# Optimization experiments

Measured on AMD Instinct MI355X. Metric: run time of the kernel, lower is better.

Reference implementation:

```python
import jax, jax.numpy as jnp
import numpy as np

EPS = 1e-5

def conv2d(x, w, padding):
    # x: (N, Cin, H, W), w: (Cout, Cin, kh, kw)
    return jax.lax.conv_general_dilated(
        x, w, window_strides=(1, 1),
        padding=[(padding, padding), (padding, padding)],
        dimension_numbers=('NCHW', 'OIHW', 'NCHW'))

def proj_bn_relu(x, w, gamma, beta, mean, var):
    # 1x1 conv + BatchNorm (eval mode, running stats) + ReLU
    y = conv2d(x, w, 0)
    scale = (gamma / jnp.sqrt(var + EPS))[None, :, None, None]
    shift = (beta - mean * gamma / jnp.sqrt(var + EPS))[None, :, None, None]
    return jax.nn.relu(y * scale + shift)

def setup_inputs() -> dict:
    key = jax.random.key(0)
    ks = jax.random.split(key, 16)
    B, Sx, Sy, C1, C2, Co, H, W, K = 2, 4, 4, 64, 64, 64, 128, 128, 3
    inp = {
        'u': jax.random.normal(ks[0], (B, Sx, C1, H, W), jnp.float32),
        'v': jax.random.normal(ks[1], (B, Sy, C2, H, W), jnp.float32),
        'pu_w': jax.random.normal(ks[2], (C1, C1, 1, 1), jnp.float32) * 0.05,
        'pu_gamma': jnp.ones((C1,), jnp.float32),
        'pu_beta': jnp.zeros((C1,), jnp.float32),
        'pu_mean': jax.random.normal(ks[3], (C1,), jnp.float32) * 0.1,
        'pu_var': jax.random.uniform(ks[4], (C1,), jnp.float32, 0.5, 1.5),
        'pv_w': jax.random.normal(ks[5], (C2, C2, 1, 1), jnp.float32) * 0.05,
        'pv_gamma': jnp.ones((C2,), jnp.float32),
        'pv_beta': jnp.zeros((C2,), jnp.float32),
        'pv_mean': jax.random.normal(ks[6], (C2,), jnp.float32) * 0.1,
        'pv_var': jax.random.uniform(ks[7], (C2,), jnp.float32, 0.5, 1.5),
        'conv_w': jax.random.normal(ks[8], (Co, C1 + C2, K, K), jnp.float32) * 0.02,
        'conv_b': jax.random.normal(ks[9], (Co,), jnp.float32) * 0.02,
    }
    return inp

def reference(u, v, pu_w, pu_gamma, pu_beta, pu_mean, pu_var,
              pv_w, pv_gamma, pv_beta, pv_mean, pv_var, conv_w, conv_b):
    B, Sx, C1, H, W = u.shape
    _, Sy, C2, _, _ = v.shape
    pad = 1
    # flatten set dims into batch for the 1x1 proj+BN+ReLU
    uf = proj_bn_relu(u.reshape(B * Sx, C1, H, W), pu_w, pu_gamma, pu_beta, pu_mean, pu_var)
    vf = proj_bn_relu(v.reshape(B * Sy, C2, H, W), pv_w, pv_gamma, pv_beta, pv_mean, pv_var)
    # conv over concat channels is linear -> split weight and broadcast-add,
    # exactly equal to conv(cat(repeat(u), repeat(v))) without materializing
    # the (B,Sx,Sy,C1+C2,H,W) tensor.
    w_u = conv_w[:, :C1]   # (Co, C1, K, K)
    w_v = conv_w[:, C1:]   # (Co, C2, K, K)
    ou = conv2d(uf, w_u, pad)  # (B*Sx, Co, Ho, Wo)
    ov = conv2d(vf, w_v, pad)  # (B*Sy, Co, Ho, Wo)
    Co, Ho, Wo = ou.shape[1], ou.shape[2], ou.shape[3]
    ou = ou.reshape(B, Sx, 1, Co, Ho, Wo)
    ov = ov.reshape(B, 1, Sy, Co, Ho, Wo)
    out = ou + ov + conv_b[None, None, None, :, None, None]
    return out  # (B, Sx, Sy, Co, Ho, Wo)
```

## Files before the change

kernel.cpp:

```cpp
#include <hip/hip_runtime.h>
#include <hip/hip_bf16.h>

#define C   64
#define Hh  128
#define Ww  128
#define HW  16384

typedef __attribute__((ext_vector_type(8))) short bf16x8;
typedef __attribute__((ext_vector_type(4))) float f32x4;

__device__ __forceinline__ unsigned short f2bf(float f) {
    unsigned u = __builtin_bit_cast(unsigned, f);
    unsigned r = (u + 0x7fff + ((u >> 16) & 1)) >> 16;
    return (unsigned short)r;
}

__global__ __launch_bounds__(256) void prep_kernel(
    const float* __restrict__ pu_w, const float* __restrict__ pu_g,
    const float* __restrict__ pu_b, const float* __restrict__ pu_m,
    const float* __restrict__ pu_v,
    const float* __restrict__ pv_w, const float* __restrict__ pv_g,
    const float* __restrict__ pv_b, const float* __restrict__ pv_m,
    const float* __restrict__ pv_v,
    const float* __restrict__ conv_w,
    short* __restrict__ pwu, short* __restrict__ pwv,
    short* __restrict__ wpu, short* __restrict__ wpv,
    float* __restrict__ shu, float* __restrict__ shv)
{
    const int idx = blockIdx.x * 256 + threadIdx.x;
    if (idx < 8192) {
        const int c  = idx >> 12;
        const int r  = idx & 4095;
        const int co = r >> 6, ci = r & 63;
        const float* w = c ? pv_w : pu_w;
        const float* g = c ? pv_g : pu_g;
        const float* vv = c ? pv_v : pu_v;
        const float scale = g[co] * rsqrtf(vv[co] + 1e-5f);
        (c ? pwv : pwu)[r] = (short)f2bf(w[co * 64 + ci] * scale);
    } else if (idx < 81920) {
        const int flat = idx - 8192;
        const int c  = flat / 36864;
        const int r  = flat % 36864;
        const int ch  = r / 18432;
        const int r2  = r % 18432;
        const int tap = r2 / 2048;
        const int r3  = r2 & 2047;
        const int co = r3 >> 5, ci = r3 & 31;
        const float src = conv_w[(size_t)(co * 128 + c * 64 + ch * 32 + ci) * 9 + tap];
        (c ? wpv : wpu)[((ch * 9 + tap) * 64 + co) * 32 + ci] = (short)f2bf(src);
    } else if (idx < 82048) {
        const int r  = idx - 81920;
        const int c  = r >> 6, co = r & 63;
        const float* g = c ? pv_g : pu_g;
        const float* b = c ? pv_b : pu_b;
        const float* m = c ? pv_m : pu_m;
        const float* vv = c ? pv_v : pu_v;
        const float scale = g[co] * rsqrtf(vv[co] + 1e-5f);
        (c ? shv : shu)[co] = b[co] - m[co] * scale;
    }
}

__global__ __launch_bounds__(256) void proj_mfma(
    const float* __restrict__ xu, const float* __restrict__ xv,
    const short* __restrict__ pwu_, const short* __restrict__ pwv_,
    const float* __restrict__ shu_, const float* __restrict__ shv_,
    short* __restrict__ yu, short* __restrict__ yv)
{
    __shared__ short xs[256 * 72];
    __shared__ short pwl[64 * 72];
    __shared__ float ssh[64];

    const int img16 = blockIdx.y;
    const int sel   = img16 >> 3;
    const int img   = img16 & 7;
    const float* x      = sel ? xv   : xu;
    const short* pw     = sel ? pwv_ : pwu_;
    const float* shiftg = sel ? shv_ : shu_;
    short* y            = sel ? yv   : yu;

    const int pix0 = blockIdx.x * 256;
    const int tid  = threadIdx.x;

    const float* xi = x + (size_t)img * C * HW + pix0 + tid;
#pragma unroll 8
    for (int c2 = 0; c2 < 32; ++c2) {
        const float a = xi[(size_t)(2 * c2) * HW];
        const float b = xi[(size_t)(2 * c2 + 1) * HW];
        const int packed = (int)f2bf(a) | ((int)f2bf(b) << 16);
        *(int*)(&xs[tid * 72 + c2 * 2]) = packed;
    }
#pragma unroll
    for (int it = 0; it < 2; ++it) {
        const int idx = tid + it * 256;
        const int oct = idx & 7, co = idx >> 3;
        *(int4*)(&pwl[co * 72 + oct * 8]) = *(const int4*)(&pw[co * 64 + oct * 8]);
    }
    if (tid < 64) ssh[tid] = shiftg[tid];
    __syncthreads();

    const int wq = tid >> 6;
    const int lane = tid & 63;
    const int lx = lane & 15;
    const int q  = lane >> 4;

    f32x4 acc[4][4];
#pragma unroll
    for (int mt = 0; mt < 4; ++mt)
#pragma unroll
        for (int nt = 0; nt < 4; ++nt) acc[mt][nt] = (f32x4){0.f, 0.f, 0.f, 0.f};

#pragma unroll
    for (int kc = 0; kc < 2; ++kc) {
        bf16x8 a[4], b[4];
#pragma unroll
        for (int mt = 0; mt < 4; ++mt)
            a[mt] = *(const bf16x8*)&xs[((wq * 4 + mt) * 16 + lx) * 72 + kc * 32 + q * 8];
#pragma unroll
        for (int nt = 0; nt < 4; ++nt)
            b[nt] = *(const bf16x8*)&pwl[(nt * 16 + lx) * 72 + kc * 32 + q * 8];
#pragma unroll
        for (int mt = 0; mt < 4; ++mt)
#pragma unroll
            for (int nt = 0; nt < 4; ++nt)
                acc[mt][nt] = __builtin_amdgcn_mfma_f32_16x16x32_bf16(a[mt], b[nt], acc[mt][nt], 0, 0, 0);
    }

    short* yo = y + ((size_t)img * HW + pix0) * C;
#pragma unroll
    for (int mt = 0; mt < 4; ++mt)
#pragma unroll
        for (int nt = 0; nt < 4; ++nt)
#pragma unroll
            for (int r = 0; r < 4; ++r) {
                const int pixl = (wq * 4 + mt) * 16 + q * 4 + r;
                const int co = nt * 16 + lx;
                float vv = acc[mt][nt][r] + ssh[co];
                vv = fmaxf(vv, 0.f);
                yo[(size_t)pixl * C + co] = (short)f2bf(vv);
            }
}

template<bool FUSED>
__global__ __launch_bounds__(256, 2) void conv_core(
    const short* __restrict__ act, const short* __restrict__ wp,
    const float* __restrict__ ou, const float* __restrict__ bias,
    float* __restrict__ outp)
{
    __shared__ short xs[340 * 40];
    __shared__ short wsm[9 * 64 * 40];
    __shared__ float sbias[64];

    const int img = blockIdx.y;
    const int tx = blockIdx.x & 3, ty = blockIdx.x >> 2;
    const int h0 = ty * 8, w0 = tx * 32;
    const int tid = threadIdx.x;
    const int wq = tid >> 6;
    const int lane = tid & 63;
    const int lx = lane & 15;
    const int q8 = (lane >> 4) * 8;

    if (FUSED && tid < 64) sbias[tid] = bias[tid];

    f32x4 acc[4][4];
#pragma unroll
    for (int mt = 0; mt < 4; ++mt)
#pragma unroll
        for (int nt = 0; nt < 4; ++nt) acc[mt][nt] = (f32x4){0.f, 0.f, 0.f, 0.f};

    const short* ub = act + (size_t)img * HW * C;

    for (int ch = 0; ch < 2; ++ch) {
        __syncthreads();
        for (int idx = tid; idx < 1360; idx += 256) {
            const int oct = idx & 3;
            const int pcell = idx >> 2;
            const int h = pcell / 34, w = pcell - h * 34;
            const int gh = h0 - 1 + h, gw = w0 - 1 + w;
            int4 v = {0, 0, 0, 0};
            if (gh >= 0 && gh < Hh && gw >= 0 && gw < Ww)
                v = *(const int4*)&ub[(size_t)(gh * Ww + gw) * C + ch * 32 + oct * 8];
            *(int4*)(&xs[pcell * 40 + oct * 8]) = v;
        }
        for (int idx = tid; idx < 2304; idx += 256) {
            const int oct = idx & 3;
            const int co = (idx >> 2) & 63;
            const int tl = idx >> 8;
            *(int4*)(&wsm[(tl * 64 + co) * 40 + oct * 8]) =
                *(const int4*)&wp[(((ch * 9 + tl) * 64) + co) * 32 + oct * 8];
        }
        __syncthreads();
#pragma unroll
        for (int t = 0; t < 9; ++t) {
            const int ky = t / 3;
            const int kx = t - ky * 3;
            bf16x8 a[4], b[4];
#pragma unroll
            for (int mt = 0; mt < 4; ++mt)
                a[mt] = *(const bf16x8*)&wsm[(t * 64 + mt * 16 + lx) * 40 + q8];
#pragma unroll
            for (int nt = 0; nt < 4; ++nt) {
                const int cell = (2 * wq + (nt >> 1) + ky) * 34 + (nt & 1) * 16 + lx + kx;
                b[nt] = *(const bf16x8*)&xs[cell * 40 + q8];
            }
#pragma unroll
            for (int mt = 0; mt < 4; ++mt)
#pragma unroll
                for (int nt = 0; nt < 4; ++nt)
                    acc[mt][nt] = __builtin_amdgcn_mfma_f32_16x16x32_bf16(a[mt], b[nt], acc[mt][nt], 0, 0, 0);
        }
    }

    const int qq = lane >> 4;
    if (!FUSED) {
        float* ob = outp + (size_t)img * C * HW;
#pragma unroll
        for (int mt = 0; mt < 4; ++mt)
#pragma unroll
            for (int nt = 0; nt < 4; ++nt)
#pragma unroll
                for (int r = 0; r < 4; ++r) {
                    const int co = mt * 16 + qq * 4 + r;
                    const int h = h0 + 2 * wq + (nt >> 1);
                    const int w = w0 + (nt & 1) * 16 + lx;
                    ob[(size_t)co * HW + h * Ww + w] = acc[mt][nt][r];
                }
    } else {
        const int b  = img >> 2;
        const int sy = img & 3;
#pragma unroll
        for (int mt = 0; mt < 4; ++mt)
#pragma unroll
            for (int nt = 0; nt < 4; ++nt)
#pragma unroll
                for (int r = 0; r < 4; ++r)
                    acc[mt][nt][r] += sbias[mt * 16 + qq * 4 + r];

#pragma unroll
        for (int sx = 0; sx < 4; ++sx) {
            const float* oub = ou + (size_t)(b * 4 + sx) * C * HW;
            float* ob = outp + ((size_t)((b * 4 + sx) * 4 + sy)) * C * HW;
#pragma unroll
            for (int mt = 0; mt < 4; ++mt)
#pragma unroll
                for (int nt = 0; nt < 4; ++nt)
#pragma unroll
                    for (int r = 0; r < 4; ++r) {
                        const int co = mt * 16 + qq * 4 + r;
                        const int h = h0 + 2 * wq + (nt >> 1);
                        const int w = w0 + (nt & 1) * 16 + lx;
                        const size_t off = (size_t)co * HW + h * Ww + w;
                        __builtin_nontemporal_store(acc[mt][nt][r] + oub[off], &ob[off]);
                    }
        }
    }
}

extern "C" void kernel_launch(void* const* d_in, const int* in_sizes, int n_in,
                              void* d_out, int out_size, void* d_ws, size_t ws_size,
                              hipStream_t stream)
{
    const float* u        = (const float*)d_in[0];
    const float* v        = (const float*)d_in[1];
    const float* pu_w     = (const float*)d_in[2];
    const float* pu_gamma = (const float*)d_in[3];
    const float* pu_beta  = (const float*)d_in[4];
    const float* pu_mean  = (const float*)d_in[5];
    const float* pu_var   = (const float*)d_in[6];
    const float* pv_w     = (const float*)d_in[7];
    const float* pv_gamma = (const float*)d_in[8];
    const float* pv_beta  = (const float*)d_in[9];
    const float* pv_mean  = (const float*)d_in[10];
    const float* pv_var   = (const float*)d_in[11];
    const float* conv_w   = (const float*)d_in[12];
    const float* conv_b   = (const float*)d_in[13];
    float* out = (float*)d_out;

    char* ws = (char*)d_ws;
    short* uf  = (short*)(ws);
    short* vf  = (short*)(ws + 16777216);
    float* ou  = (float*)(ws + 33554432);
    char*  aux = ws + 100663296;
    short* pwu = (short*)(aux);
    short* pwv = (short*)(aux + 8192);
    short* wpu = (short*)(aux + 16384);
    short* wpv = (short*)(aux + 90112);
    float* shu = (float*)(aux + 163840);
    float* shv = (float*)(aux + 164096);

    prep_kernel<<<321, 256, 0, stream>>>(pu_w, pu_gamma, pu_beta, pu_mean, pu_var,
                                         pv_w, pv_gamma, pv_beta, pv_mean, pv_var,
                                         conv_w, pwu, pwv, wpu, wpv, shu, shv);

    dim3 gp(64, 16);
    proj_mfma<<<gp, 256, 0, stream>>>(u, v, pwu, pwv, shu, shv, uf, vf);

    dim3 gc(64, 8);
    conv_core<false><<<gc, 256, 0, stream>>>(uf, wpu, nullptr, nullptr, ou);
    conv_core<true ><<<gc, 256, 0, stream>>>(vf, wpv, ou, conv_b, out);
}
```

Measured before the change: 262.7 us.

## Fuse 1x1 projection+BN+ReLU into the 3x3 conv kernel via halo recompute

Removes the separate projection kernel and its bf16 intermediate activations. Each conv block now loads fp32 input for its 10x34 halo tile, computes the 1x1 projection with MFMA into shared memory, and zeroes out-of-image padding before running the 3x3 conv from that buffer. The conv weights are staged in three smaller per-row groups to fit the larger activation tile in LDS, and the projection weights use an XOR-swizzled layout. This trades extra halo recomputation, more barriers and higher LDS use per block for removing one launch and a full round-trip of the intermediate through global memory.

```diff
diff --git a/kernel.cpp b/kernel.cpp
--- a/kernel.cpp
+++ b/kernel.cpp
@@ -60,94 +60,17 @@
     }
 }
 
-__global__ __launch_bounds__(256) void proj_mfma(
-    const float* __restrict__ xu, const float* __restrict__ xv,
-    const short* __restrict__ pwu_, const short* __restrict__ pwv_,
-    const float* __restrict__ shu_, const float* __restrict__ shv_,
-    short* __restrict__ yu, short* __restrict__ yv)
-{
-    __shared__ short xs[256 * 72];
-    __shared__ short pwl[64 * 72];
-    __shared__ float ssh[64];
-
-    const int img16 = blockIdx.y;
-    const int sel   = img16 >> 3;
-    const int img   = img16 & 7;
-    const float* x      = sel ? xv   : xu;
-    const short* pw     = sel ? pwv_ : pwu_;
-    const float* shiftg = sel ? shv_ : shu_;
-    short* y            = sel ? yv   : yu;
-
-    const int pix0 = blockIdx.x * 256;
-    const int tid  = threadIdx.x;
-
-    const float* xi = x + (size_t)img * C * HW + pix0 + tid;
-#pragma unroll 8
-    for (int c2 = 0; c2 < 32; ++c2) {
-        const float a = xi[(size_t)(2 * c2) * HW];
-        const float b = xi[(size_t)(2 * c2 + 1) * HW];
-        const int packed = (int)f2bf(a) | ((int)f2bf(b) << 16);
-        *(int*)(&xs[tid * 72 + c2 * 2]) = packed;
-    }
-#pragma unroll
-    for (int it = 0; it < 2; ++it) {
-        const int idx = tid + it * 256;
-        const int oct = idx & 7, co = idx >> 3;
-        *(int4*)(&pwl[co * 72 + oct * 8]) = *(const int4*)(&pw[co * 64 + oct * 8]);
-    }
-    if (tid < 64) ssh[tid] = shiftg[tid];
-    __syncthreads();
-
-    const int wq = tid >> 6;
-    const int lane = tid & 63;
-    const int lx = lane & 15;
-    const int q  = lane >> 4;
-
-    f32x4 acc[4][4];
-#pragma unroll
-    for (int mt = 0; mt < 4; ++mt)
-#pragma unroll
-        for (int nt = 0; nt < 4; ++nt) acc[mt][nt] = (f32x4){0.f, 0.f, 0.f, 0.f};
-
-#pragma unroll
-    for (int kc = 0; kc < 2; ++kc) {
-        bf16x8 a[4], b[4];
-#pragma unroll
-        for (int mt = 0; mt < 4; ++mt)
-            a[mt] = *(const bf16x8*)&xs[((wq * 4 + mt) * 16 + lx) * 72 + kc * 32 + q * 8];
-#pragma unroll
-        for (int nt = 0; nt < 4; ++nt)
-            b[nt] = *(const bf16x8*)&pwl[(nt * 16 + lx) * 72 + kc * 32 + q * 8];
-#pragma unroll
-        for (int mt = 0; mt < 4; ++mt)
-#pragma unroll
-            for (int nt = 0; nt < 4; ++nt)
-                acc[mt][nt] = __builtin_amdgcn_mfma_f32_16x16x32_bf16(a[mt], b[nt], acc[mt][nt], 0, 0, 0);
-    }
-
-    short* yo = y + ((size_t)img * HW + pix0) * C;
-#pragma unroll
-    for (int mt = 0; mt < 4; ++mt)
-#pragma unroll
-        for (int nt = 0; nt < 4; ++nt)
-#pragma unroll
-            for (int r = 0; r < 4; ++r) {
-                const int pixl = (wq * 4 + mt) * 16 + q * 4 + r;
-                const int co = nt * 16 + lx;
-                float vv = acc[mt][nt][r] + ssh[co];
-                vv = fmaxf(vv, 0.f);
-                yo[(size_t)pixl * C + co] = (short)f2bf(vv);
-            }
-}
-
 template<bool FUSED>
-__global__ __launch_bounds__(256, 2) void conv_core(
-    const short* __restrict__ act, const short* __restrict__ wp,
-    const float* __restrict__ ou, const float* __restrict__ bias,
+__global__ __launch_bounds__(256, 2) void fused_pc(
+    const float* __restrict__ xg, const short* __restrict__ pw,
+    const float* __restrict__ shg, const short* __restrict__ wp,
+    const float* __restrict__ oug, const float* __restrict__ bias,
     float* __restrict__ outp)
 {
-    __shared__ short xs[340 * 40];
-    __shared__ short wsm[9 * 64 * 40];
+    __shared__ short xs2[384 * 68];
+    __shared__ short wsm[3 * 64 * 40];
+    __shared__ short pwl[64 * 64];
+    __shared__ float ssh[64];
     __shared__ float sbias[64];
 
     const int img = blockIdx.y;
@@ -157,9 +80,80 @@
     const int wq = tid >> 6;
     const int lane = tid & 63;
     const int lx = lane & 15;
-    const int q8 = (lane >> 4) * 8;
-
-    if (FUSED && tid < 64) sbias[tid] = bias[tid];
+    const int q  = lane >> 4;
+
+#pragma unroll
+    for (int it = 0; it < 2; ++it) {
+        const int idx = tid + it * 256;
+        const int oct = idx & 7, co = idx >> 3;
+        *(int4*)&pwl[co * 64 + ((oct * 8) ^ ((co & 7) << 3))] =
+            *(const int4*)&pw[co * 64 + oct * 8];
+    }
+    if (tid < 64) ssh[tid] = shg[tid];
+    if (FUSED && tid >= 64 && tid < 128) sbias[tid - 64] = bias[tid - 64];
+#pragma unroll
+    for (int it = 0; it < 3; ++it) {
+        const int idx = tid + it * 256;
+        const int oct = idx & 3, co = (idx >> 2) & 63, tl = idx >> 8;
+        *(int4*)&wsm[(tl * 64 + co) * 40 + oct * 8] =
+            *(const int4*)&wp[(tl * 64 + co) * 32 + oct * 8];
+    }
+    const float* xb = xg + (size_t)img * C * HW;
+    for (int idx = tid; idx < 10880; idx += 256) {
+        const int p = idx / 340;
+        const int cell = idx - p * 340;
+        const int h = cell / 34, w2 = cell - h * 34;
+        const int gh = h0 - 1 + h, gw = w0 - 1 + w2;
+        int packed = 0;
+        if (gh >= 0 && gh < Hh && gw >= 0 && gw < Ww) {
+            const float* s = xb + (size_t)(2 * p) * HW + gh * Ww + gw;
+            packed = (int)f2bf(s[0]) | ((int)f2bf(s[HW]) << 16);
+        }
+        *(int*)&xs2[cell * 68 + p * 2] = packed;
+    }
+    __syncthreads();
+
+    f32x4 pacc[6][4];
+#pragma unroll
+    for (int mt = 0; mt < 6; ++mt)
+#pragma unroll
+        for (int nt = 0; nt < 4; ++nt) pacc[mt][nt] = (f32x4){0.f, 0.f, 0.f, 0.f};
+
+#pragma unroll
+    for (int kc = 0; kc < 2; ++kc) {
+        bf16x8 pa[6], pb[4];
+#pragma unroll
+        for (int mt = 0; mt < 6; ++mt)
+            pa[mt] = *(const bf16x8*)&xs2[((wq * 6 + mt) * 16 + lx) * 68 + kc * 32 + q * 8];
+#pragma unroll
+        for (int nt = 0; nt < 4; ++nt) {
+            const int row = nt * 16 + lx;
+            const int off = kc * 32 + q * 8;
+            pb[nt] = *(const bf16x8*)&pwl[row * 64 + (off ^ ((row & 7) << 3))];
+        }
+#pragma unroll
+        for (int mt = 0; mt < 6; ++mt)
+#pragma unroll
+            for (int nt = 0; nt < 4; ++nt)
+                pacc[mt][nt] = __builtin_amdgcn_mfma_f32_16x16x32_bf16(pa[mt], pb[nt], pacc[mt][nt], 0, 0, 0);
+    }
+    __syncthreads();
+#pragma unroll
+    for (int mt = 0; mt < 6; ++mt)
+#pragma unroll
+        for (int r = 0; r < 4; ++r) {
+            const int px = (wq * 6 + mt) * 16 + q * 4 + r;
+            const int h = px / 34, w2 = px - h * 34;
+            const int gh = h0 - 1 + h, gw = w0 - 1 + w2;
+            const bool ok = (gh >= 0) && (gh < Hh) && (gw >= 0) && (gw < Ww) && (px < 340);
+#pragma unroll
+            for (int nt = 0; nt < 4; ++nt) {
+                const int co = nt * 16 + lx;
+                const float vv = ok ? fmaxf(pacc[mt][nt][r] + ssh[co], 0.f) : 0.f;
+                xs2[px * 68 + co] = (short)f2bf(vv);
+            }
+        }
+    __syncthreads();
 
     f32x4 acc[4][4];
 #pragma unroll
@@ -167,46 +161,34 @@
 #pragma unroll
         for (int nt = 0; nt < 4; ++nt) acc[mt][nt] = (f32x4){0.f, 0.f, 0.f, 0.f};
 
-    const short* ub = act + (size_t)img * HW * C;
-
     for (int ch = 0; ch < 2; ++ch) {
-        __syncthreads();
-        for (int idx = tid; idx < 1360; idx += 256) {
-            const int oct = idx & 3;
-            const int pcell = idx >> 2;
-            const int h = pcell / 34, w = pcell - h * 34;
-            const int gh = h0 - 1 + h, gw = w0 - 1 + w;
-            int4 v = {0, 0, 0, 0};
-            if (gh >= 0 && gh < Hh && gw >= 0 && gw < Ww)
-                v = *(const int4*)&ub[(size_t)(gh * Ww + gw) * C + ch * 32 + oct * 8];
-            *(int4*)(&xs[pcell * 40 + oct * 8]) = v;
-        }
-        for (int idx = tid; idx < 2304; idx += 256) {
-            const int oct = idx & 3;
-            const int co = (idx >> 2) & 63;
-            const int tl = idx >> 8;
-            *(int4*)(&wsm[(tl * 64 + co) * 40 + oct * 8]) =
-                *(const int4*)&wp[(((ch * 9 + tl) * 64) + co) * 32 + oct * 8];
-        }
-        __syncthreads();
-#pragma unroll
-        for (int t = 0; t < 9; ++t) {
-            const int ky = t / 3;
-            const int kx = t - ky * 3;
-            bf16x8 a[4], b[4];
-#pragma unroll
-            for (int mt = 0; mt < 4; ++mt)
-                a[mt] = *(const bf16x8*)&wsm[(t * 64 + mt * 16 + lx) * 40 + q8];
-#pragma unroll
-            for (int nt = 0; nt < 4; ++nt) {
-                const int cell = (2 * wq + (nt >> 1) + ky) * 34 + (nt & 1) * 16 + lx + kx;
-                b[nt] = *(const bf16x8*)&xs[cell * 40 + q8];
+        for (int g = 0; g < 3; ++g) {
+            if (ch | g) {
+                __syncthreads();
+                for (int idx = tid; idx < 768; idx += 256) {
+                    const int oct = idx & 3, co = (idx >> 2) & 63, tl = idx >> 8;
+                    *(int4*)&wsm[(tl * 64 + co) * 40 + oct * 8] =
+                        *(const int4*)&wp[((ch * 9 + g * 3 + tl) * 64 + co) * 32 + oct * 8];
+                }
+                __syncthreads();
             }
 #pragma unroll
-            for (int mt = 0; mt < 4; ++mt)
-#pragma unroll
-                for (int nt = 0; nt < 4; ++nt)
-                    acc[mt][nt] = __builtin_amdgcn_mfma_f32_16x16x32_bf16(a[mt], b[nt], acc[mt][nt], 0, 0, 0);
+            for (int tl = 0; tl < 3; ++tl) {
+                bf16x8 a[4], b[4];
+#pragma unroll
+                for (int mt = 0; mt < 4; ++mt)
+                    a[mt] = *(const bf16x8*)&wsm[(tl * 64 + mt * 16 + lx) * 40 + q * 8];
+#pragma unroll
+                for (int nt = 0; nt < 4; ++nt) {
+                    const int cell = (2 * wq + (nt >> 1) + g) * 34 + (nt & 1) * 16 + lx + tl;
+                    b[nt] = *(const bf16x8*)&xs2[cell * 68 + ch * 32 + q * 8];
+                }
+#pragma unroll
+                for (int mt = 0; mt < 4; ++mt)
+#pragma unroll
+                    for (int nt = 0; nt < 4; ++nt)
+                        acc[mt][nt] = __builtin_amdgcn_mfma_f32_16x16x32_bf16(a[mt], b[nt], acc[mt][nt], 0, 0, 0);
+            }
         }
     }
 
@@ -237,7 +219,7 @@
 
 #pragma unroll
         for (int sx = 0; sx < 4; ++sx) {
-            const float* oub = ou + (size_t)(b * 4 + sx) * C * HW;
+            const float* oub = oug + (size_t)(b * 4 + sx) * C * HW;
             float* ob = outp + ((size_t)((b * 4 + sx) * 4 + sy)) * C * HW;
 #pragma unroll
             for (int mt = 0; mt < 4; ++mt)
@@ -276,10 +258,8 @@
     float* out = (float*)d_out;
 
     char* ws = (char*)d_ws;
-    short* uf  = (short*)(ws);
-    short* vf  = (short*)(ws + 16777216);
-    float* ou  = (float*)(ws + 33554432);
-    char*  aux = ws + 100663296;
+    float* ou  = (float*)(ws);
+    char*  aux = ws + 33554432;
     short* pwu = (short*)(aux);
     short* pwv = (short*)(aux + 8192);
     short* wpu = (short*)(aux + 16384);
@@ -291,10 +271,7 @@
                                          pv_w, pv_gamma, pv_beta, pv_mean, pv_var,
                                          conv_w, pwu, pwv, wpu, wpv, shu, shv);
 
-    dim3 gp(64, 16);
-    proj_mfma<<<gp, 256, 0, stream>>>(u, v, pwu, pwv, shu, shv, uf, vf);
-
     dim3 gc(64, 8);
-    conv_core<false><<<gc, 256, 0, stream>>>(uf, wpu, nullptr, nullptr, ou);
-    conv_core<true ><<<gc, 256, 0, stream>>>(vf, wpv, ou, conv_b, out);
-}
+    fused_pc<false><<<gc, 256, 0, stream>>>(u, pwu, shu, wpu, nullptr, nullptr, ou);
+    fused_pc<true ><<<gc, 256, 0, stream>>>(v, pwv, shv, wpv, ou, conv_b, out);
+}
```

Result: slower. 291.9 us (+11.1%).

## Coalesce conv and projection stores via LDS staging, halve conv tile height

Applied to the files above, without the earlier changes.

The projection kernel now stages its bf16 outputs in shared memory and writes them as 16-byte vectors instead of scattered 2-byte stores. The conv kernel uses 4-row tiles, loads all 64 channels of the halo tile once, reads weights directly from global/L1 instead of staging them in LDS, and transposes accumulators through LDS so output and ou reads/writes become float4 coalesced accesses. Occupancy hints are raised, to 4 blocks per CU for conv and 3 for proj, and the grid doubles. The risks are extra LDS round trips and syncs, and weight reads from global memory that may go uncached.

```diff
diff --git a/kernel.cpp b/kernel.cpp
--- a/kernel.cpp
+++ b/kernel.cpp
@@ -60,7 +60,7 @@
     }
 }
 
-__global__ __launch_bounds__(256) void proj_mfma(
+__global__ __launch_bounds__(256, 3) void proj_mfma(
     const float* __restrict__ xu, const float* __restrict__ xv,
     const short* __restrict__ pwu_, const short* __restrict__ pwv_,
     const float* __restrict__ shu_, const float* __restrict__ shv_,
@@ -125,132 +125,142 @@
                 acc[mt][nt] = __builtin_amdgcn_mfma_f32_16x16x32_bf16(a[mt], b[nt], acc[mt][nt], 0, 0, 0);
     }
 
-    short* yo = y + ((size_t)img * HW + pix0) * C;
+    __syncthreads();
 #pragma unroll
     for (int mt = 0; mt < 4; ++mt)
 #pragma unroll
         for (int nt = 0; nt < 4; ++nt)
 #pragma unroll
             for (int r = 0; r < 4; ++r) {
-                const int pixl = (wq * 4 + mt) * 16 + q * 4 + r;
+                const int px = (wq * 4 + mt) * 16 + q * 4 + r;
                 const int co = nt * 16 + lx;
                 float vv = acc[mt][nt][r] + ssh[co];
                 vv = fmaxf(vv, 0.f);
-                yo[(size_t)pixl * C + co] = (short)f2bf(vv);
+                xs[px * 72 + co] = (short)f2bf(vv);
             }
+    __syncthreads();
+    short* yo = y + ((size_t)img * HW + pix0) * C;
+#pragma unroll
+    for (int it = 0; it < 8; ++it) {
+        const int idx = tid + it * 256;
+        const int oct = idx & 7, px = idx >> 3;
+        *(int4*)&yo[(size_t)px * C + oct * 8] = *(const int4*)&xs[px * 72 + oct * 8];
+    }
 }
 
 template<bool FUSED>
-__global__ __launch_bounds__(256, 2) void conv_core(
+__global__ __launch_bounds__(256, 4) void conv_fused(
     const short* __restrict__ act, const short* __restrict__ wp,
-    const float* __restrict__ ou, const float* __restrict__ bias,
+    const float* __restrict__ oug, const float* __restrict__ bias,
     float* __restrict__ outp)
 {
-    __shared__ short xs[340 * 40];
-    __shared__ short wsm[9 * 64 * 40];
+    __shared__ short xs[204 * 68];
+    __shared__ float ts[16 * 132];
     __shared__ float sbias[64];
 
     const int img = blockIdx.y;
     const int tx = blockIdx.x & 3, ty = blockIdx.x >> 2;
-    const int h0 = ty * 8, w0 = tx * 32;
+    const int h0 = ty * 4, w0 = tx * 32;
     const int tid = threadIdx.x;
     const int wq = tid >> 6;
     const int lane = tid & 63;
     const int lx = lane & 15;
-    const int q8 = (lane >> 4) * 8;
+    const int q  = lane >> 4;
+    const int q8 = q * 8;
 
     if (FUSED && tid < 64) sbias[tid] = bias[tid];
 
-    f32x4 acc[4][4];
+    const short* ub = act + (size_t)img * HW * C;
+    for (int idx = tid; idx < 1632; idx += 256) {
+        const int oct = idx & 7;
+        const int cell = idx >> 3;
+        const int h = cell / 34, w = cell - h * 34;
+        const int gh = h0 - 1 + h, gw = w0 - 1 + w;
+        int4 v = {0, 0, 0, 0};
+        if (gh >= 0 && gh < Hh && gw >= 0 && gw < Ww)
+            v = *(const int4*)&ub[(size_t)(gh * Ww + gw) * C + oct * 8];
+        *(int4*)(&xs[cell * 68 + oct * 8]) = v;
+    }
+    __syncthreads();
+
+    f32x4 acc[4][2];
 #pragma unroll
     for (int mt = 0; mt < 4; ++mt)
 #pragma unroll
-        for (int nt = 0; nt < 4; ++nt) acc[mt][nt] = (f32x4){0.f, 0.f, 0.f, 0.f};
-
-    const short* ub = act + (size_t)img * HW * C;
-
-    for (int ch = 0; ch < 2; ++ch) {
-        __syncthreads();
-        for (int idx = tid; idx < 1360; idx += 256) {
-            const int oct = idx & 3;
-            const int pcell = idx >> 2;
-            const int h = pcell / 34, w = pcell - h * 34;
-            const int gh = h0 - 1 + h, gw = w0 - 1 + w;
-            int4 v = {0, 0, 0, 0};
-            if (gh >= 0 && gh < Hh && gw >= 0 && gw < Ww)
-                v = *(const int4*)&ub[(size_t)(gh * Ww + gw) * C + ch * 32 + oct * 8];
-            *(int4*)(&xs[pcell * 40 + oct * 8]) = v;
-        }
-        for (int idx = tid; idx < 2304; idx += 256) {
-            const int oct = idx & 3;
-            const int co = (idx >> 2) & 63;
-            const int tl = idx >> 8;
-            *(int4*)(&wsm[(tl * 64 + co) * 40 + oct * 8]) =
-                *(const int4*)&wp[(((ch * 9 + tl) * 64) + co) * 32 + oct * 8];
-        }
-        __syncthreads();
+        for (int nt = 0; nt < 2; ++nt) acc[mt][nt] = (f32x4){0.f, 0.f, 0.f, 0.f};
+
+#pragma unroll
+    for (int ch = 0; ch < 2; ++ch)
 #pragma unroll
         for (int t = 0; t < 9; ++t) {
             const int ky = t / 3;
             const int kx = t - ky * 3;
-            bf16x8 a[4], b[4];
+            bf16x8 a[4], b[2];
 #pragma unroll
             for (int mt = 0; mt < 4; ++mt)
-                a[mt] = *(const bf16x8*)&wsm[(t * 64 + mt * 16 + lx) * 40 + q8];
-#pragma unroll
-            for (int nt = 0; nt < 4; ++nt) {
-                const int cell = (2 * wq + (nt >> 1) + ky) * 34 + (nt & 1) * 16 + lx + kx;
-                b[nt] = *(const bf16x8*)&xs[cell * 40 + q8];
+                a[mt] = *(const bf16x8*)&wp[(((ch * 9 + t) * 64) + mt * 16 + lx) * 32 + q8];
+#pragma unroll
+            for (int nt = 0; nt < 2; ++nt) {
+                const int cell = (wq + ky) * 34 + nt * 16 + lx + kx;
+                b[nt] = *(const bf16x8*)&xs[cell * 68 + ch * 32 + q8];
             }
 #pragma unroll
             for (int mt = 0; mt < 4; ++mt)
 #pragma unroll
-                for (int nt = 0; nt < 4; ++nt)
+                for (int nt = 0; nt < 2; ++nt)
                     acc[mt][nt] = __builtin_amdgcn_mfma_f32_16x16x32_bf16(a[mt], b[nt], acc[mt][nt], 0, 0, 0);
         }
-    }
-
-    const int qq = lane >> 4;
-    if (!FUSED) {
-        float* ob = outp + (size_t)img * C * HW;
+
+    if (FUSED) {
 #pragma unroll
         for (int mt = 0; mt < 4; ++mt)
 #pragma unroll
-            for (int nt = 0; nt < 4; ++nt)
-#pragma unroll
-                for (int r = 0; r < 4; ++r) {
-                    const int co = mt * 16 + qq * 4 + r;
-                    const int h = h0 + 2 * wq + (nt >> 1);
-                    const int w = w0 + (nt & 1) * 16 + lx;
-                    ob[(size_t)co * HW + h * Ww + w] = acc[mt][nt][r];
+            for (int nt = 0; nt < 2; ++nt)
+#pragma unroll
+                for (int r = 0; r < 4; ++r)
+                    acc[mt][nt][r] += sbias[mt * 16 + q * 4 + r];
+    }
+
+    const int b  = img >> 2;
+    const int sy = img & 3;
+
+#pragma unroll
+    for (int mt = 0; mt < 4; ++mt) {
+        __syncthreads();
+#pragma unroll
+        for (int nt = 0; nt < 2; ++nt)
+#pragma unroll
+            for (int r = 0; r < 4; ++r)
+                ts[(q * 4 + r) * 132 + wq * 32 + nt * 16 + lx] = acc[mt][nt][r];
+        __syncthreads();
+        if (!FUSED) {
+            float* ob = outp + (size_t)img * C * HW;
+#pragma unroll
+            for (int k = 0; k < 2; ++k) {
+                const int f = tid + k * 256;
+                const int co = f >> 5, c2 = f & 31;
+                const int px = c2 * 4;
+                const int h2 = px >> 5, w2 = px & 31;
+                *(f32x4*)&ob[(size_t)(mt * 16 + co) * HW + (h0 + h2) * Ww + w0 + w2] =
+                    *(const f32x4*)&ts[co * 132 + c2 * 4];
+            }
+        } else {
+#pragma unroll
+            for (int k = 0; k < 2; ++k) {
+                const int f = tid + k * 256;
+                const int co = f >> 5, c2 = f & 31;
+                const int px = c2 * 4;
+                const int h2 = px >> 5, w2 = px & 31;
+                const size_t off = (size_t)(mt * 16 + co) * HW + (h0 + h2) * Ww + w0 + w2;
+                const f32x4 tv = *(const f32x4*)&ts[co * 132 + c2 * 4];
+#pragma unroll
+                for (int sx = 0; sx < 4; ++sx) {
+                    const f32x4 o = *(const f32x4*)&oug[(size_t)(b * 4 + sx) * C * HW + off];
+                    f32x4 rr = tv + o;
+                    __builtin_nontemporal_store(rr,
+                        (f32x4*)&outp[((size_t)((b * 4 + sx) * 4 + sy)) * C * HW + off]);
                 }
-    } else {
-        const int b  = img >> 2;
-        const int sy = img & 3;
-#pragma unroll
-        for (int mt = 0; mt < 4; ++mt)
-#pragma unroll
-            for (int nt = 0; nt < 4; ++nt)
-#pragma unroll
-                for (int r = 0; r < 4; ++r)
-                    acc[mt][nt][r] += sbias[mt * 16 + qq * 4 + r];
-
-#pragma unroll
-        for (int sx = 0; sx < 4; ++sx) {
-            const float* oub = ou + (size_t)(b * 4 + sx) * C * HW;
-            float* ob = outp + ((size_t)((b * 4 + sx) * 4 + sy)) * C * HW;
-#pragma unroll
-            for (int mt = 0; mt < 4; ++mt)
-#pragma unroll
-                for (int nt = 0; nt < 4; ++nt)
-#pragma unroll
-                    for (int r = 0; r < 4; ++r) {
-                        const int co = mt * 16 + qq * 4 + r;
-                        const int h = h0 + 2 * wq + (nt >> 1);
-                        const int w = w0 + (nt & 1) * 16 + lx;
-                        const size_t off = (size_t)co * HW + h * Ww + w;
-                        __builtin_nontemporal_store(acc[mt][nt][r] + oub[off], &ob[off]);
-                    }
+            }
         }
     }
 }
@@ -279,7 +289,7 @@
     short* uf  = (short*)(ws);
     short* vf  = (short*)(ws + 16777216);
     float* ou  = (float*)(ws + 33554432);
-    char*  aux = ws + 100663296;
+    char*  aux = ws + 67108864;
     short* pwu = (short*)(aux);
     short* pwv = (short*)(aux + 8192);
     short* wpu = (short*)(aux + 16384);
@@ -294,7 +304,7 @@
     dim3 gp(64, 16);
     proj_mfma<<<gp, 256, 0, stream>>>(u, v, pwu, pwv, shu, shv, uf, vf);
 
-    dim3 gc(64, 8);
-    conv_core<false><<<gc, 256, 0, stream>>>(uf, wpu, nullptr, nullptr, ou);
-    conv_core<true ><<<gc, 256, 0, stream>>>(vf, wpv, ou, conv_b, out);
-}
+    dim3 gc(128, 8);
+    conv_fused<false><<<gc, 256, 0, stream>>>(uf, wpu, nullptr, nullptr, ou);
+    conv_fused<true ><<<gc, 256, 0, stream>>>(vf, wpv, ou, conv_b, out);
+}
```

Result: no change. 263.6 us (+0.3%).
